# Kernel tuning notes

Measured on AMD Instinct MI355X. Metric: run time of the kernel, lower is better.

The kernel has to match this reference:

```python
import jax, jax.numpy as jnp
import numpy as np

N = 50000          # nodes
E = 1250000        # edges (no self loops in raw data)
H = 2              # heads
C = 32             # out channels per head
DIN = 64           # dim_node
ED = 16            # edge_dim
G = 16             # graphs in batch
NC = 5             # num classes
SLOPE = 0.2        # GATConv leaky_relu negative_slope


def _glorot(key, shape):
    fan = shape[0] if len(shape) == 2 else shape[-1]
    return jax.random.normal(key, shape, jnp.float32) * (1.0 / np.sqrt(fan))


def setup_inputs() -> dict:
    key = jax.random.key(0)
    ks = jax.random.split(key, 24)
    x = jax.random.normal(ks[0], (N, DIN), jnp.float32)
    dst = jax.random.randint(ks[1], (E,), 0, N)
    off = jax.random.randint(ks[2], (E,), 1, N)
    src = (dst + off) % N  # guarantees src != dst (PyG removes self loops before re-adding)
    edge_index = jnp.stack([src, dst]).astype(jnp.int32)
    edge_attr = jax.random.normal(ks[3], (E, ED), jnp.float32)
    batch = jnp.sort(jax.random.randint(ks[4], (N,), 0, G)).astype(jnp.int32)
    inp = dict(x=x, edge_index=edge_index, edge_attr=edge_attr, batch=batch)
    # layer 1: in=DIN, heads=H, out=C, concat -> H*C
    inp["W1"] = _glorot(ks[5], (DIN, H * C)); inp["asrc1"] = _glorot(ks[6], (H, C))
    inp["adst1"] = _glorot(ks[7], (H, C)); inp["We1"] = _glorot(ks[8], (ED, H * C))
    inp["ae1"] = _glorot(ks[9], (H, C)); inp["b1"] = jnp.zeros((H * C,), jnp.float32)
    # layer 2: in=H*C, heads=H, out=C, concat
    inp["W2"] = _glorot(ks[10], (H * C, H * C)); inp["asrc2"] = _glorot(ks[11], (H, C))
    inp["adst2"] = _glorot(ks[12], (H, C)); inp["We2"] = _glorot(ks[13], (ED, H * C))
    inp["ae2"] = _glorot(ks[14], (H, C)); inp["b2"] = jnp.zeros((H * C,), jnp.float32)
    # layer 3: in=H*C, heads=1, out=C, concat=False
    inp["W3"] = _glorot(ks[15], (H * C, C)); inp["asrc3"] = _glorot(ks[16], (1, C))
    inp["adst3"] = _glorot(ks[17], (1, C)); inp["We3"] = _glorot(ks[18], (ED, C))
    inp["ae3"] = _glorot(ks[19], (1, C)); inp["b3"] = jnp.zeros((C,), jnp.float32)
    # ffn: Linear(C, NC) + softmax (dropout is identity in eval)
    inp["Wf"] = _glorot(ks[20], (C, NC)); inp["bf"] = jnp.zeros((NC,), jnp.float32)
    return inp


def _gat_layer(h_in, src, dst, eattr, W, asrc, adst, We, ae, b, heads, out, concat):
    n = h_in.shape[0]
    h = (h_in @ W).reshape(n, heads, out)                      # [N,H,C]
    s_src = jnp.einsum('nhc,hc->nh', h, asrc)                  # per-node src scores
    s_dst = jnp.einsum('nhc,hc->nh', h, adst)
    he = (eattr @ We).reshape(-1, heads, out)                  # [E,H,C]
    s_e = jnp.einsum('ehc,hc->eh', he, ae)
    logit = jax.nn.leaky_relu(s_src[src] + s_dst[dst] + s_e, SLOPE)  # [E,H]
    m = jax.ops.segment_max(logit, dst, num_segments=n)
    ex = jnp.exp(logit - m[dst])
    den = jax.ops.segment_sum(ex, dst, num_segments=n)
    alpha = ex / (den[dst] + 1e-16)                            # segment softmax per dst node
    agg = jax.ops.segment_sum(h[src] * alpha[..., None], dst, num_segments=n)  # [N,H,C]
    out_x = agg.reshape(n, heads * out) if concat else agg.mean(axis=1)
    return out_x + b


def _gat_forward(x, edge_index, edge_attr, batch,
                 W1, asrc1, adst1, We1, ae1, b1,
                 W2, asrc2, adst2, We2, ae2, b2,
                 W3, asrc3, adst3, We3, ae3, b3,
                 Wf, bf):
    src, dst = edge_index[0], edge_index[1]
    n = x.shape[0]
    # add_self_loops with fill_value='mean': self-loop edge_attr = mean of incoming edge_attr
    deg = jax.ops.segment_sum(jnp.ones((src.shape[0],), x.dtype), dst, num_segments=n)
    self_attr = jax.ops.segment_sum(edge_attr, dst, num_segments=n) / jnp.maximum(deg, 1.0)[:, None]
    loop = jnp.arange(n, dtype=src.dtype)
    src_a = jnp.concatenate([src, loop])
    dst_a = jnp.concatenate([dst, loop])
    eattr_a = jnp.concatenate([edge_attr, self_attr], axis=0)

    h = jax.nn.relu(_gat_layer(x, src_a, dst_a, eattr_a, W1, asrc1, adst1, We1, ae1, b1, H, C, True))
    h = jax.nn.relu(_gat_layer(h, src_a, dst_a, eattr_a, W2, asrc2, adst2, We2, ae2, b2, H, C, True))
    h = jax.nn.relu(_gat_layer(h, src_a, dst_a, eattr_a, W3, asrc3, adst3, We3, ae3, b3, 1, C, False))

    # global mean pool per graph
    cnt = jax.ops.segment_sum(jnp.ones((n,), h.dtype), batch, num_segments=G)
    pooled = jax.ops.segment_sum(h, batch, num_segments=G) / jnp.maximum(cnt, 1.0)[:, None]
    # ffn: Dropout (identity at eval) -> Linear -> Softmax(dim=1)
    return jax.nn.softmax(pooled @ Wf + bf, axis=1)


def reference(x, edge_index, edge_attr, batch,
              W1, asrc1, adst1, We1, ae1, b1,
              W2, asrc2, adst2, We2, ae2, b2,
              W3, asrc3, adst3, We3, ae3, b3,
              Wf, bf):
    return _gat_forward(x, edge_index, edge_attr, batch,
                        W1, asrc1, adst1, We1, ae1, b1,
                        W2, asrc2, adst2, We2, ae2, b2,
                        W3, asrc3, adst3, We3, ae3, b3,
                        Wf, bf)
```

## Files before the change

### kernel.cpp

```cpp
#include <hip/hip_runtime.h>
#include <math.h>

#define NN 50000
#define EE 1250000
#define GG 16
#define NCLS 5
#define NBIN 391
#define BINSHIFT 7
#define CAPB 3900

constexpr size_t AL(size_t x){ return (x + 255) & ~size_t(255); }
constexpr size_t OFF_DEG    = 0;
constexpr size_t OFF_ROWPTR = OFF_DEG + AL((size_t)NN*4);
constexpr size_t OFF_CURSOR = OFF_ROWPTR + AL((size_t)(NN+1)*4);
constexpr size_t OFF_SRCS   = OFF_CURSOR + AL((size_t)NN*4);
constexpr size_t OFF_SE12   = OFF_SRCS + AL((size_t)EE*2);
constexpr size_t OFF_SE34   = OFF_SE12 + AL((size_t)EE*4);
constexpr size_t OFF_SE5    = OFF_SE34 + AL((size_t)EE*4);
constexpr size_t OFF_SSRC   = OFF_SE5 + AL((size_t)EE*2);
constexpr size_t OFF_SDST   = OFF_SSRC + AL((size_t)NN*2*4);
constexpr size_t OFF_STAG   = OFF_SDST + AL((size_t)NN*2*4);
constexpr size_t OFF_BUFH   = OFF_STAG + AL((size_t)NBIN*CAPB*16);
constexpr size_t OFF_BUFO   = OFF_BUFH + AL((size_t)NN*32*4);
constexpr size_t OFF_WEFF   = OFF_BUFO + AL((size_t)NN*64*4);
constexpr size_t OFF_POOL   = OFF_WEFF + AL(80*4);

__device__ __forceinline__ float leaky(float x){ return x > 0.f ? x : 0.2f*x; }
__device__ __forceinline__ unsigned rne_bf16(float x){
    unsigned u = __float_as_uint(x);
    return (u + 0x7FFFu + ((u >> 16) & 1u)) >> 16;
}
__device__ __forceinline__ float bf16lo(unsigned p){ return __uint_as_float(p << 16); }
__device__ __forceinline__ float bf16hi(unsigned p){ return __uint_as_float(p & 0xFFFF0000u); }

__global__ void weff_kernel(const float* __restrict__ We1, const float* __restrict__ ae1,
                            const float* __restrict__ We2, const float* __restrict__ ae2,
                            const float* __restrict__ We3, const float* __restrict__ ae3,
                            float* __restrict__ weff){
    int t = threadIdx.x;
    if (t >= 80) return;
    int j = t >> 4, d = t & 15;
    const float* We; const float* ae; int hc, h;
    if (j == 0){ We = We1; ae = ae1; hc = 64; h = 0; }
    else if (j == 1){ We = We1; ae = ae1; hc = 64; h = 1; }
    else if (j == 2){ We = We2; ae = ae2; hc = 64; h = 0; }
    else if (j == 3){ We = We2; ae = ae2; hc = 64; h = 1; }
    else { We = We3; ae = ae3; hc = 32; h = 0; }
    float s = 0.f;
    for (int c = 0; c < 32; ++c) s += We[d*hc + h*32 + c] * ae[h*32 + c];
    weff[j*16 + d] = s;
}

__global__ void binit_kernel(int* __restrict__ bincursor){
    int b = blockIdx.x*256 + threadIdx.x;
    if (b < NBIN) bincursor[b] = b*CAPB;
}

__global__ void binA_kernel(const int* __restrict__ src, const int* __restrict__ dst,
                            const float* __restrict__ eattr, const float* __restrict__ weff,
                            int* __restrict__ bincursor, int4* __restrict__ staging, int nE){
    __shared__ int lcount[NBIN];
    __shared__ int lbase[NBIN];
    __shared__ float w[80];
    int tid = threadIdx.x;
    if (tid < 80) w[tid] = weff[tid];
    for (int i = tid; i < NBIN; i += 1024) lcount[i] = 0;
    __syncthreads();
    int base = blockIdx.x * 2048;
    int w0[2], bn[2], idx[2]; unsigned p01[2], p23[2], p4[2];
    #pragma unroll
    for (int k = 0; k < 2; ++k){
        int i = base + k*1024 + tid;
        if (i < nE){
            int d = dst[i];
            int s = src[i];
            bn[k]  = d >> BINSHIFT;
            w0[k]  = s | ((d & 127) << 16);
            const float4* row = (const float4*)(eattr + (size_t)i*16);
            float4 a0 = row[0], a1 = row[1], a2 = row[2], a3 = row[3];
            float a[16] = {a0.x,a0.y,a0.z,a0.w, a1.x,a1.y,a1.z,a1.w,
                           a2.x,a2.y,a2.z,a2.w, a3.x,a3.y,a3.z,a3.w};
            float sj[5];
            #pragma unroll
            for (int j = 0; j < 5; ++j){
                float s2 = 0.f;
                #pragma unroll
                for (int d2 = 0; d2 < 16; ++d2) s2 += a[d2]*w[j*16+d2];
                sj[j] = s2;
            }
            p01[k] = rne_bf16(sj[0]) | (rne_bf16(sj[1]) << 16);
            p23[k] = rne_bf16(sj[2]) | (rne_bf16(sj[3]) << 16);
            p4[k]  = rne_bf16(sj[4]);
            idx[k] = atomicAdd(&lcount[bn[k]], 1);
        } else bn[k] = -1;
    }
    __syncthreads();
    for (int i = tid; i < NBIN; i += 1024)
        lbase[i] = atomicAdd(&bincursor[i], lcount[i]);
    __syncthreads();
    #pragma unroll
    for (int k = 0; k < 2; ++k)
        if (bn[k] >= 0)
            staging[lbase[bn[k]] + idx[k]] = make_int4(w0[k], (int)p01[k], (int)p23[k], (int)p4[k]);
}

__global__ void hist_kernel(const int4* __restrict__ staging, const int* __restrict__ bincursor,
                            int* __restrict__ deg, int nN){
    __shared__ int lcnt[128];
    int b = blockIdx.x;
    int tid = threadIdx.x;
    if (tid < 128) lcnt[tid] = 0;
    __syncthreads();
    int base = b*CAPB;
    int cnt = bincursor[b] - base;
    for (int k = tid; k < cnt; k += 256)
        atomicAdd(&lcnt[staging[base + k].x >> 16], 1);
    __syncthreads();
    int lo = b << BINSHIFT;
    if (tid < 128 && lo + tid < nN) deg[lo + tid] = lcnt[tid];
}

__global__ void bsum_kernel(const int* __restrict__ deg, int* __restrict__ bsum, int nN){
    __shared__ int s[1024];
    int tid = threadIdx.x;
    int i = blockIdx.x*1024 + tid;
    s[tid] = (i < nN) ? deg[i] : 0;
    __syncthreads();
    for (int off = 512; off > 0; off >>= 1){
        if (tid < off) s[tid] += s[tid+off];
        __syncthreads();
    }
    if (tid == 0) bsum[blockIdx.x] = s[0];
}

__global__ void bscan_kernel(const int* __restrict__ bsum, int* __restrict__ boff,
                             int* __restrict__ rowptr, int nB, int nN){
    int lane = threadIdx.x;
    int v = (lane < nB) ? bsum[lane] : 0;
    int incl = v;
    #pragma unroll
    for (int off = 1; off < 64; off <<= 1){
        int t = __shfl_up(incl, off);
        if (lane >= off) incl += t;
    }
    if (lane < nB) boff[lane] = incl - v;
    if (lane == 63) rowptr[nN] = incl;
}

__global__ void wptr_kernel(const int* __restrict__ deg, const int* __restrict__ boff,
                            int* __restrict__ rowptr, int nN){
    __shared__ int s[1024];
    int tid = threadIdx.x;
    int i = blockIdx.x*1024 + tid;
    int v = (i < nN) ? deg[i] : 0;
    s[tid] = v;
    __syncthreads();
    for (int off = 1; off < 1024; off <<= 1){
        int t = (tid >= off) ? s[tid-off] : 0;
        __syncthreads();
        s[tid] += t;
        __syncthreads();
    }
    if (i < nN) rowptr[i] = boff[blockIdx.x] + s[tid] - v;
}

__global__ void binB_kernel(const int* __restrict__ rowptr, const int4* __restrict__ staging,
                            unsigned short* __restrict__ srcs, unsigned* __restrict__ se12,
                            unsigned* __restrict__ se34, unsigned short* __restrict__ se5, int nN){
    __shared__ int4 lout[CAPB];
    __shared__ int lcnt[128];
    int b = blockIdx.x;
    int lo = b << BINSHIFT;
    int hi = min(lo + 128, nN);
    int r0 = rowptr[lo], r1 = rowptr[hi];
    int cnt = r1 - r0;
    int sbase = b*CAPB;
    int tid = threadIdx.x;
    if (tid < 128) lcnt[tid] = 0;
    __syncthreads();
    for (int k = tid; k < cnt; k += 1024){
        int4 v = staging[sbase + k];
        int dl = v.x >> 16;
        int rank = atomicAdd(&lcnt[dl], 1);
        int target = rowptr[lo + dl] - r0 + rank;
        v.x &= 0xFFFF;
        if (target < CAPB) lout[target] = v;
        else {
            srcs[r0 + target] = (unsigned short)v.x;
            se12[r0 + target] = (unsigned)v.y;
            se34[r0 + target] = (unsigned)v.z;
            se5[r0 + target]  = (unsigned short)v.w;
        }
    }
    __syncthreads();
    int m = min(cnt, CAPB);
    for (int k = tid; k < m; k += 1024){
        int4 v = lout[k];
        srcs[r0 + k] = (unsigned short)v.x;
        se12[r0 + k] = (unsigned)v.y;
        se34[r0 + k] = (unsigned)v.z;
        se5[r0 + k]  = (unsigned short)v.w;
    }
}

template<int OUTC>
__global__ void transform_kernel(const float* __restrict__ in, const float* __restrict__ W,
                                 const float* __restrict__ asrc, const float* __restrict__ adst,
                                 unsigned* __restrict__ hout2, float* __restrict__ ssrc,
                                 float* __restrict__ sdst, int nN){
    constexpr int R = 256/OUTC;
    __shared__ float Ws[64*OUTC];
    __shared__ float ins[R*64];
    int tid = threadIdx.x;
    for (int i = tid; i < 64*OUTC; i += 256) Ws[i] = W[i];
    int base = blockIdx.x * R;
    for (int i = tid; i < R*64; i += 256){
        int n = base + i/64;
        ins[i] = (n < nN) ? in[(size_t)n*64 + (i & 63)] : 0.f;
    }
    __syncthreads();
    int r = tid / OUTC, c = tid % OUTC;
    int n = base + r;
    float acc = 0.f;
    #pragma unroll
    for (int d = 0; d < 64; ++d) acc += ins[r*64 + d] * Ws[d*OUTC + c];
    float ps = acc * asrc[c];
    float pd = acc * adst[c];
    #pragma unroll
    for (int m = 1; m <= 16; m <<= 1){ ps += __shfl_xor(ps, m); pd += __shfl_xor(pd, m); }
    float accN = __shfl_xor(acc, 1);
    if (n < nN){
        if ((c & 1) == 0){
            unsigned pk = rne_bf16(acc) | (rne_bf16(accN) << 16);
            hout2[(size_t)n*(OUTC/2) + (c >> 1)] = pk;
        }
        constexpr int HEADS = OUTC/32;
        if ((c & 31) == 0){
            int h = c >> 5;
            ssrc[n*HEADS + h] = ps;
            sdst[n*HEADS + h] = pd;
        }
    }
}

template<int OUTC>
__global__ void agg_kernel(const int* __restrict__ rowptr, const unsigned short* __restrict__ srcs,
                           const unsigned* __restrict__ sePa, const unsigned short* __restrict__ sePb,
                           const float* __restrict__ ssrc, const float* __restrict__ sdst,
                           const unsigned* __restrict__ hbuf2, const float* __restrict__ bias,
                           float* __restrict__ outbuf, int nN){
    constexpr int HEADS = OUTC/32;
    int wid = threadIdx.x >> 6;
    int lane = threadIdx.x & 63;
    int n = blockIdx.x*4 + wid;
    if (n >= nN) return;
    int row_start = rowptr[n], row_end = rowptr[n+1];
    int degn = row_end - row_start;
    float sd0 = sdst[n*HEADS + 0];
    float sd1 = (HEADS == 2) ? sdst[n*HEADS + 1] : 0.f;

    const uint2* hb2 = (const uint2*)hbuf2;
    float acc0=0.f, acc1=0.f, acc2=0.f, acc3=0.f, den=0.f, sspL=0.f;

    int h, lc;
    if (HEADS == 2){ int s = lane >> 3; h = s & 1; lc = lane & 7; }
    else           { h = 0; lc = lane & 7; }

    if (HEADS == 2){
        int eoff = lane >> 1, hp = lane & 1;
        int q0 = (lane >> 4);
        float sdh_p = hp ? sd1 : sd0;
        for (int p0 = row_start; p0 < row_end; p0 += 32){
            int myp = p0 + eoff;
            unsigned wpk = 0;
            if (myp < row_end){
                int srcreg = srcs[myp];
                unsigned pk = sePa[myp];
                float e = hp ? bf16hi(pk) : bf16lo(pk);
                sspL += e;
                float sh = ssrc[2*srcreg + hp];
                float wv = __expf(leaky(sh + sdh_p + e));
                wpk = (unsigned)srcreg | (rne_bf16(wv) << 16);
            }
            int cnt = min(32, row_end - p0);
            for (int qq = q0; qq < cnt; qq += 4){
                unsigned u = __shfl(wpk, 2*qq + h);
                int sj = u & 0xFFFF;
                float wj = __uint_as_float(u & 0xFFFF0000u);
                den += wj;
                uint2 hv = hb2[(size_t)sj*16 + h*8 + lc];
                acc0 += wj * bf16lo(hv.x);
                acc1 += wj * bf16hi(hv.x);
                acc2 += wj * bf16lo(hv.y);
                acc3 += wj * bf16hi(hv.y);
            }
        }
        #pragma unroll
        for (int m = 2; m < 64; m <<= 1) sspL += __shfl_xor(sspL, m);
        float ssh = __shfl(sspL, h);
        #pragma unroll
        for (int m = 16; m < 64; m <<= 1){
            acc0 += __shfl_xor(acc0, m); acc1 += __shfl_xor(acc1, m);
            acc2 += __shfl_xor(acc2, m); acc3 += __shfl_xor(acc3, m);
            den  += __shfl_xor(den, m);
        }
        float invdeg = 1.f / (float)max(degn, 1);
        float srh = ssrc[2*n + h];
        float sdh = h ? sd1 : sd0;
        float wself = __expf(leaky(srh + sdh + ssh*invdeg));
        uint2 hv = hb2[(size_t)n*16 + h*8 + lc];
        acc0 += wself * bf16lo(hv.x); acc1 += wself * bf16hi(hv.x);
        acc2 += wself * bf16lo(hv.y); acc3 += wself * bf16hi(hv.y);
        den += wself;
        if (lane < 16){
            float inv = 1.f / (den + 1e-16f);
            int idx4 = h*8 + lc;
            float4 o;
            o.x = fmaxf(acc0*inv + bias[4*idx4+0], 0.f);
            o.y = fmaxf(acc1*inv + bias[4*idx4+1], 0.f);
            o.z = fmaxf(acc2*inv + bias[4*idx4+2], 0.f);
            o.w = fmaxf(acc3*inv + bias[4*idx4+3], 0.f);
            ((float4*)outbuf)[(size_t)n*16 + idx4] = o;
        }
    } else {
        int q0 = lane >> 3;
        for (int p0 = row_start; p0 < row_end; p0 += 64){
            int myp = p0 + lane;
            unsigned wpk = 0;
            if (myp < row_end){
                int srcreg = srcs[myp];
                float e = __uint_as_float(((unsigned)sePb[myp]) << 16);
                sspL += e;
                float wv = __expf(leaky(ssrc[srcreg] + sd0 + e));
                wpk = (unsigned)srcreg | (rne_bf16(wv) << 16);
            }
            int cnt = min(64, row_end - p0);
            for (int qq = q0; qq < cnt; qq += 8){
                unsigned u = __shfl(wpk, qq);
                int sj = u & 0xFFFF;
                float wj = __uint_as_float(u & 0xFFFF0000u);
                den += wj;
                uint2 hv = hb2[(size_t)sj*8 + lc];
                acc0 += wj * bf16lo(hv.x);
                acc1 += wj * bf16hi(hv.x);
                acc2 += wj * bf16lo(hv.y);
                acc3 += wj * bf16hi(hv.y);
            }
        }
        #pragma unroll
        for (int m = 1; m < 64; m <<= 1) sspL += __shfl_xor(sspL, m);
        float ssh = sspL;
        #pragma unroll
        for (int m = 8; m < 64; m <<= 1){
            acc0 += __shfl_xor(acc0, m); acc1 += __shfl_xor(acc1, m);
            acc2 += __shfl_xor(acc2, m); acc3 += __shfl_xor(acc3, m);
            den  += __shfl_xor(den, m);
        }
        float invdeg = 1.f / (float)max(degn, 1);
        float wself = __expf(leaky(ssrc[n] + sd0 + ssh*invdeg));
        uint2 hv = hb2[(size_t)n*8 + lc];
        acc0 += wself * bf16lo(hv.x); acc1 += wself * bf16hi(hv.x);
        acc2 += wself * bf16lo(hv.y); acc3 += wself * bf16hi(hv.y);
        den += wself;
        if (lane < 8){
            float inv = 1.f / (den + 1e-16f);
            float4 o;
            o.x = fmaxf(acc0*inv + bias[4*lc+0], 0.f);
            o.y = fmaxf(acc1*inv + bias[4*lc+1], 0.f);
            o.z = fmaxf(acc2*inv + bias[4*lc+2], 0.f);
            o.w = fmaxf(acc3*inv + bias[4*lc+3], 0.f);
            ((float4*)outbuf)[(size_t)n*8 + lc] = o;
        }
    }
}

__global__ void pool_kernel(const float* __restrict__ h3, const int* __restrict__ batch,
                            float* __restrict__ pool, float* __restrict__ cnt, int nN){
    __shared__ float accs[GG*32];
    __shared__ float acccnt[GG];
    int tid = threadIdx.x;
    for (int i = tid; i < GG*32; i += 256) accs[i] = 0.f;
    if (tid < GG) acccnt[tid] = 0.f;
    __syncthreads();
    int r = tid >> 5, c = tid & 31;
    int base = blockIdx.x * 512;
    int end = min(base + 512, nN);
    for (int n = base + r; n < end; n += 8){
        int g = batch[n];
        atomicAdd(&accs[g*32 + c], h3[(size_t)n*32 + c]);
        if (c == 0) atomicAdd(&acccnt[g], 1.f);
    }
    __syncthreads();
    for (int i = tid; i < GG*32; i += 256) atomicAdd(&pool[i], accs[i]);
    if (tid < GG) atomicAdd(&cnt[tid], acccnt[tid]);
}

__global__ void final_kernel(const float* __restrict__ pool, const float* __restrict__ cnt,
                             const float* __restrict__ Wf, const float* __restrict__ bf,
                             float* __restrict__ out){
    int g = threadIdx.x;
    if (g >= GG) return;
    float ic = 1.f / fmaxf(cnt[g], 1.f);
    float lg[NCLS];
    #pragma unroll
    for (int k = 0; k < NCLS; ++k) lg[k] = bf[k];
    for (int c = 0; c < 32; ++c){
        float v = pool[g*32 + c] * ic;
        #pragma unroll
        for (int k = 0; k < NCLS; ++k) lg[k] += v * Wf[c*NCLS + k];
    }
    float mx = lg[0];
    #pragma unroll
    for (int k = 1; k < NCLS; ++k) mx = fmaxf(mx, lg[k]);
    float sum = 0.f, ex[NCLS];
    #pragma unroll
    for (int k = 0; k < NCLS; ++k){ ex[k] = expf(lg[k] - mx); sum += ex[k]; }
    #pragma unroll
    for (int k = 0; k < NCLS; ++k) out[g*NCLS + k] = ex[k]/sum;
}

extern "C" void kernel_launch(void* const* d_in, const int* in_sizes, int n_in,
                              void* d_out, int out_size, void* d_ws, size_t ws_size,
                              hipStream_t stream){
    const float* x     = (const float*)d_in[0];
    const int*   eidx  = (const int*)d_in[1];
    const float* eattr = (const float*)d_in[2];
    const int*   batch = (const int*)d_in[3];
    const float* W1 = (const float*)d_in[4];  const float* asrc1 = (const float*)d_in[5];
    const float* adst1 = (const float*)d_in[6]; const float* We1 = (const float*)d_in[7];
    const float* ae1 = (const float*)d_in[8];  const float* b1 = (const float*)d_in[9];
    const float* W2 = (const float*)d_in[10]; const float* asrc2 = (const float*)d_in[11];
    const float* adst2 = (const float*)d_in[12]; const float* We2 = (const float*)d_in[13];
    const float* ae2 = (const float*)d_in[14]; const float* b2 = (const float*)d_in[15];
    const float* W3 = (const float*)d_in[16]; const float* asrc3 = (const float*)d_in[17];
    const float* adst3 = (const float*)d_in[18]; const float* We3 = (const float*)d_in[19];
    const float* ae3 = (const float*)d_in[20]; const float* b3 = (const float*)d_in[21];
    const float* Wf = (const float*)d_in[22]; const float* bf = (const float*)d_in[23];
    float* out = (float*)d_out;

    char* ws = (char*)d_ws;
    int*   deg    = (int*)(ws + OFF_DEG);
    int*   rowptr = (int*)(ws + OFF_ROWPTR);
    int*   curs   = (int*)(ws + OFF_CURSOR);
    unsigned short* srcs = (unsigned short*)(ws + OFF_SRCS);
    unsigned* se12 = (unsigned*)(ws + OFF_SE12);
    unsigned* se34 = (unsigned*)(ws + OFF_SE34);
    unsigned short* se5 = (unsigned short*)(ws + OFF_SE5);
    float* ssrc   = (float*)(ws + OFF_SSRC);
    float* sdst   = (float*)(ws + OFF_SDST);
    int4*  staging = (int4*)(ws + OFF_STAG);
    unsigned* bufH = (unsigned*)(ws + OFF_BUFH);
    float* bufO   = (float*)(ws + OFF_BUFO);
    float* weff   = (float*)(ws + OFF_WEFF);
    float* pool   = (float*)(ws + OFF_POOL);
    float* cnt    = pool + GG*32;

    int* bincursor = curs;
    int* bsum      = curs + 512;
    int* boff      = curs + 1024;

    const int* srcA = eidx;
    const int* dstA = eidx + EE;

    hipMemsetAsync(pool, 0, (GG*32 + GG)*4, stream);

    weff_kernel<<<1, 128, 0, stream>>>(We1, ae1, We2, ae2, We3, ae3, weff);
    binit_kernel<<<(NBIN+255)/256, 256, 0, stream>>>(bincursor);
    binA_kernel<<<(EE + 2047)/2048, 1024, 0, stream>>>(srcA, dstA, eattr, weff, bincursor, staging, EE);
    hist_kernel<<<NBIN, 256, 0, stream>>>(staging, bincursor, deg, NN);
    int sgrid = (NN + 1023)/1024;
    bsum_kernel<<<sgrid, 1024, 0, stream>>>(deg, bsum, NN);
    bscan_kernel<<<1, 64, 0, stream>>>(bsum, boff, rowptr, sgrid, NN);
    wptr_kernel<<<sgrid, 1024, 0, stream>>>(deg, boff, rowptr, NN);
    binB_kernel<<<NBIN, 1024, 0, stream>>>(rowptr, staging, srcs, se12, se34, se5, NN);

    int ngrid4 = (NN + 3)/4;
    int ngrid8 = (NN + 7)/8;
    transform_kernel<64><<<ngrid4, 256, 0, stream>>>(x, W1, asrc1, adst1, bufH, ssrc, sdst, NN);
    agg_kernel<64><<<ngrid4, 256, 0, stream>>>(rowptr, srcs, se12, nullptr,
                                               ssrc, sdst, bufH, b1, bufO, NN);
    transform_kernel<64><<<ngrid4, 256, 0, stream>>>(bufO, W2, asrc2, adst2, bufH, ssrc, sdst, NN);
    agg_kernel<64><<<ngrid4, 256, 0, stream>>>(rowptr, srcs, se34, nullptr,
                                               ssrc, sdst, bufH, b2, bufO, NN);
    transform_kernel<32><<<ngrid8, 256, 0, stream>>>(bufO, W3, asrc3, adst3, bufH, ssrc, sdst, NN);
    agg_kernel<32><<<ngrid4, 256, 0, stream>>>(rowptr, srcs, nullptr, se5,
                                               ssrc, sdst, bufH, b3, bufO, NN);
    pool_kernel<<<(NN + 511)/512, 256, 0, stream>>>(bufO, batch, pool, cnt, NN);
    final_kernel<<<1, 64, 0, stream>>>(pool, cnt, Wf, bf, out);
}
```

Baseline: 275.8 us.

## Fuse CSR build into bin kernels and split aggregation per head with head-major layout

Derives rowptr from per-bin counts inside binB, computing a local histogram and prefix scan there and prefix-summing bin totals in one small kernel. This replaces the separate hist/bsum/bscan/wptr kernels and the deg buffer, and merges binit into weff. The transform output and attention scores are stored head-major. Aggregation runs as one kernel per head, so each gather touches a contiguous per-head slice with a single code path. Layers 1 and 2 now launch twice as many aggregation kernels and re-read the CSR once per head.

```diff
diff --git a/kernel.cpp b/kernel.cpp
--- a/kernel.cpp
+++ b/kernel.cpp
@@ -10,10 +10,9 @@
 #define CAPB 3900
 
 constexpr size_t AL(size_t x){ return (x + 255) & ~size_t(255); }
-constexpr size_t OFF_DEG    = 0;
-constexpr size_t OFF_ROWPTR = OFF_DEG + AL((size_t)NN*4);
-constexpr size_t OFF_CURSOR = OFF_ROWPTR + AL((size_t)(NN+1)*4);
-constexpr size_t OFF_SRCS   = OFF_CURSOR + AL((size_t)NN*4);
+constexpr size_t OFF_ROWPTR = 0;
+constexpr size_t OFF_CURS   = OFF_ROWPTR + AL((size_t)(NN+1)*4);
+constexpr size_t OFF_SRCS   = OFF_CURS + AL(4096);
 constexpr size_t OFF_SE12   = OFF_SRCS + AL((size_t)EE*2);
 constexpr size_t OFF_SE34   = OFF_SE12 + AL((size_t)EE*4);
 constexpr size_t OFF_SE5    = OFF_SE34 + AL((size_t)EE*4);
@@ -33,11 +32,12 @@
 __device__ __forceinline__ float bf16lo(unsigned p){ return __uint_as_float(p << 16); }
 __device__ __forceinline__ float bf16hi(unsigned p){ return __uint_as_float(p & 0xFFFF0000u); }
 
-__global__ void weff_kernel(const float* __restrict__ We1, const float* __restrict__ ae1,
-                            const float* __restrict__ We2, const float* __restrict__ ae2,
-                            const float* __restrict__ We3, const float* __restrict__ ae3,
-                            float* __restrict__ weff){
+__global__ void weffbinit_kernel(const float* __restrict__ We1, const float* __restrict__ ae1,
+                                 const float* __restrict__ We2, const float* __restrict__ ae2,
+                                 const float* __restrict__ We3, const float* __restrict__ ae3,
+                                 float* __restrict__ weff, int* __restrict__ bincursor){
     int t = threadIdx.x;
+    if (t < NBIN) bincursor[t] = t*CAPB;
     if (t >= 80) return;
     int j = t >> 4, d = t & 15;
     const float* We; const float* ae; int hc, h;
@@ -49,11 +49,6 @@
     float s = 0.f;
     for (int c = 0; c < 32; ++c) s += We[d*hc + h*32 + c] * ae[h*32 + c];
     weff[j*16 + d] = s;
-}
-
-__global__ void binit_kernel(int* __restrict__ bincursor){
-    int b = blockIdx.x*256 + threadIdx.x;
-    if (b < NBIN) bincursor[b] = b*CAPB;
 }
 
 __global__ void binA_kernel(const int* __restrict__ src, const int* __restrict__ dst,
@@ -104,97 +99,66 @@
             staging[lbase[bn[k]] + idx[k]] = make_int4(w0[k], (int)p01[k], (int)p23[k], (int)p4[k]);
 }
 
-__global__ void hist_kernel(const int4* __restrict__ staging, const int* __restrict__ bincursor,
-                            int* __restrict__ deg, int nN){
-    __shared__ int lcnt[128];
-    int b = blockIdx.x;
-    int tid = threadIdx.x;
-    if (tid < 128) lcnt[tid] = 0;
-    __syncthreads();
-    int base = b*CAPB;
-    int cnt = bincursor[b] - base;
-    for (int k = tid; k < cnt; k += 256)
-        atomicAdd(&lcnt[staging[base + k].x >> 16], 1);
-    __syncthreads();
-    int lo = b << BINSHIFT;
-    if (tid < 128 && lo + tid < nN) deg[lo + tid] = lcnt[tid];
-}
-
-__global__ void bsum_kernel(const int* __restrict__ deg, int* __restrict__ bsum, int nN){
-    __shared__ int s[1024];
-    int tid = threadIdx.x;
-    int i = blockIdx.x*1024 + tid;
-    s[tid] = (i < nN) ? deg[i] : 0;
-    __syncthreads();
-    for (int off = 512; off > 0; off >>= 1){
-        if (tid < off) s[tid] += s[tid+off];
-        __syncthreads();
-    }
-    if (tid == 0) bsum[blockIdx.x] = s[0];
-}
-
-__global__ void bscan_kernel(const int* __restrict__ bsum, int* __restrict__ boff,
-                             int* __restrict__ rowptr, int nB, int nN){
-    int lane = threadIdx.x;
-    int v = (lane < nB) ? bsum[lane] : 0;
-    int incl = v;
-    #pragma unroll
-    for (int off = 1; off < 64; off <<= 1){
-        int t = __shfl_up(incl, off);
-        if (lane >= off) incl += t;
-    }
-    if (lane < nB) boff[lane] = incl - v;
-    if (lane == 63) rowptr[nN] = incl;
-}
-
-__global__ void wptr_kernel(const int* __restrict__ deg, const int* __restrict__ boff,
-                            int* __restrict__ rowptr, int nN){
-    __shared__ int s[1024];
-    int tid = threadIdx.x;
-    int i = blockIdx.x*1024 + tid;
-    int v = (i < nN) ? deg[i] : 0;
+__global__ void binscan_kernel(const int* __restrict__ bincursor, int* __restrict__ binbase){
+    __shared__ int s[512];
+    int tid = threadIdx.x;
+    int v = (tid < NBIN) ? (bincursor[tid] - tid*CAPB) : 0;
     s[tid] = v;
     __syncthreads();
-    for (int off = 1; off < 1024; off <<= 1){
+    for (int off = 1; off < 512; off <<= 1){
         int t = (tid >= off) ? s[tid-off] : 0;
         __syncthreads();
         s[tid] += t;
         __syncthreads();
     }
-    if (i < nN) rowptr[i] = boff[blockIdx.x] + s[tid] - v;
-}
-
-__global__ void binB_kernel(const int* __restrict__ rowptr, const int4* __restrict__ staging,
+    if (tid < NBIN) binbase[tid] = s[tid] - v;
+}
+
+__global__ void binB_kernel(const int* __restrict__ bincursor, const int* __restrict__ binbase,
+                            const int4* __restrict__ staging,
                             unsigned short* __restrict__ srcs, unsigned* __restrict__ se12,
-                            unsigned* __restrict__ se34, unsigned short* __restrict__ se5, int nN){
+                            unsigned* __restrict__ se34, unsigned short* __restrict__ se5,
+                            int* __restrict__ rowptr, int nN){
     __shared__ int4 lout[CAPB];
     __shared__ int lcnt[128];
+    __shared__ int lpre[128];
     int b = blockIdx.x;
+    int sbase = b*CAPB;
+    int cnt = bincursor[b] - sbase;
+    int tid = threadIdx.x;
+    if (tid < 128) lcnt[tid] = 0;
+    __syncthreads();
+    for (int k = tid; k < cnt; k += 1024)
+        atomicAdd(&lcnt[staging[sbase + k].x >> 16], 1);
+    __syncthreads();
+    if (tid < 64){
+        int a0 = lcnt[2*tid], a1 = lcnt[2*tid+1];
+        int pair = a0 + a1, incl = pair;
+        #pragma unroll
+        for (int off = 1; off < 64; off <<= 1){
+            int t = __shfl_up(incl, off);
+            if (tid >= off) incl += t;
+        }
+        int base0 = incl - pair;
+        lpre[2*tid] = base0;
+        lpre[2*tid+1] = base0 + a0;
+    }
+    __syncthreads();
+    int r0 = binbase[b];
     int lo = b << BINSHIFT;
-    int hi = min(lo + 128, nN);
-    int r0 = rowptr[lo], r1 = rowptr[hi];
-    int cnt = r1 - r0;
-    int sbase = b*CAPB;
-    int tid = threadIdx.x;
+    if (tid < 128 && lo + tid < nN) rowptr[lo + tid] = r0 + lpre[tid];
+    if (b == NBIN-1 && tid == 0) rowptr[nN] = r0 + cnt;
     if (tid < 128) lcnt[tid] = 0;
     __syncthreads();
     for (int k = tid; k < cnt; k += 1024){
         int4 v = staging[sbase + k];
         int dl = v.x >> 16;
         int rank = atomicAdd(&lcnt[dl], 1);
-        int target = rowptr[lo + dl] - r0 + rank;
         v.x &= 0xFFFF;
-        if (target < CAPB) lout[target] = v;
-        else {
-            srcs[r0 + target] = (unsigned short)v.x;
-            se12[r0 + target] = (unsigned)v.y;
-            se34[r0 + target] = (unsigned)v.z;
-            se5[r0 + target]  = (unsigned short)v.w;
-        }
-    }
-    __syncthreads();
-    int m = min(cnt, CAPB);
-    for (int k = tid; k < m; k += 1024){
+        lout[lpre[dl] + rank] = v;
+    }
+    __syncthreads();
+    for (int k = tid; k < cnt; k += 1024){
         int4 v = lout[k];
         srcs[r0 + k] = (unsigned short)v.x;
         se12[r0 + k] = (unsigned)v.y;
@@ -230,147 +194,82 @@
     for (int m = 1; m <= 16; m <<= 1){ ps += __shfl_xor(ps, m); pd += __shfl_xor(pd, m); }
     float accN = __shfl_xor(acc, 1);
     if (n < nN){
+        int h = c >> 5;
         if ((c & 1) == 0){
             unsigned pk = rne_bf16(acc) | (rne_bf16(accN) << 16);
-            hout2[(size_t)n*(OUTC/2) + (c >> 1)] = pk;
-        }
-        constexpr int HEADS = OUTC/32;
+            hout2[((size_t)h*nN + n)*16 + ((c & 31) >> 1)] = pk;
+        }
         if ((c & 31) == 0){
-            int h = c >> 5;
-            ssrc[n*HEADS + h] = ps;
-            sdst[n*HEADS + h] = pd;
-        }
-    }
-}
-
-template<int OUTC>
-__global__ void agg_kernel(const int* __restrict__ rowptr, const unsigned short* __restrict__ srcs,
-                           const unsigned* __restrict__ sePa, const unsigned short* __restrict__ sePb,
-                           const float* __restrict__ ssrc, const float* __restrict__ sdst,
-                           const unsigned* __restrict__ hbuf2, const float* __restrict__ bias,
-                           float* __restrict__ outbuf, int nN){
-    constexpr int HEADS = OUTC/32;
+            ssrc[(size_t)h*nN + n] = ps;
+            sdst[(size_t)h*nN + n] = pd;
+        }
+    }
+}
+
+template<int MODE>
+__global__ void aggH_kernel(const int* __restrict__ rowptr, const unsigned short* __restrict__ srcs,
+                            const unsigned* __restrict__ sePa, const unsigned short* __restrict__ sePb,
+                            const float* __restrict__ ssrcH, const float* __restrict__ sdstH,
+                            const uint2* __restrict__ hb2, const float* __restrict__ bias,
+                            float4* __restrict__ outb, int ostride4, int nN){
     int wid = threadIdx.x >> 6;
     int lane = threadIdx.x & 63;
     int n = blockIdx.x*4 + wid;
     if (n >= nN) return;
     int row_start = rowptr[n], row_end = rowptr[n+1];
     int degn = row_end - row_start;
-    float sd0 = sdst[n*HEADS + 0];
-    float sd1 = (HEADS == 2) ? sdst[n*HEADS + 1] : 0.f;
-
-    const uint2* hb2 = (const uint2*)hbuf2;
-    float acc0=0.f, acc1=0.f, acc2=0.f, acc3=0.f, den=0.f, sspL=0.f;
-
-    int h, lc;
-    if (HEADS == 2){ int s = lane >> 3; h = s & 1; lc = lane & 7; }
-    else           { h = 0; lc = lane & 7; }
-
-    if (HEADS == 2){
-        int eoff = lane >> 1, hp = lane & 1;
-        int q0 = (lane >> 4);
-        float sdh_p = hp ? sd1 : sd0;
-        for (int p0 = row_start; p0 < row_end; p0 += 32){
-            int myp = p0 + eoff;
-            unsigned wpk = 0;
-            if (myp < row_end){
-                int srcreg = srcs[myp];
-                unsigned pk = sePa[myp];
-                float e = hp ? bf16hi(pk) : bf16lo(pk);
-                sspL += e;
-                float sh = ssrc[2*srcreg + hp];
-                float wv = __expf(leaky(sh + sdh_p + e));
-                wpk = (unsigned)srcreg | (rne_bf16(wv) << 16);
-            }
-            int cnt = min(32, row_end - p0);
-            for (int qq = q0; qq < cnt; qq += 4){
-                unsigned u = __shfl(wpk, 2*qq + h);
-                int sj = u & 0xFFFF;
-                float wj = __uint_as_float(u & 0xFFFF0000u);
-                den += wj;
-                uint2 hv = hb2[(size_t)sj*16 + h*8 + lc];
-                acc0 += wj * bf16lo(hv.x);
-                acc1 += wj * bf16hi(hv.x);
-                acc2 += wj * bf16lo(hv.y);
-                acc3 += wj * bf16hi(hv.y);
-            }
-        }
-        #pragma unroll
-        for (int m = 2; m < 64; m <<= 1) sspL += __shfl_xor(sspL, m);
-        float ssh = __shfl(sspL, h);
-        #pragma unroll
-        for (int m = 16; m < 64; m <<= 1){
-            acc0 += __shfl_xor(acc0, m); acc1 += __shfl_xor(acc1, m);
-            acc2 += __shfl_xor(acc2, m); acc3 += __shfl_xor(acc3, m);
-            den  += __shfl_xor(den, m);
-        }
-        float invdeg = 1.f / (float)max(degn, 1);
-        float srh = ssrc[2*n + h];
-        float sdh = h ? sd1 : sd0;
-        float wself = __expf(leaky(srh + sdh + ssh*invdeg));
-        uint2 hv = hb2[(size_t)n*16 + h*8 + lc];
-        acc0 += wself * bf16lo(hv.x); acc1 += wself * bf16hi(hv.x);
-        acc2 += wself * bf16lo(hv.y); acc3 += wself * bf16hi(hv.y);
-        den += wself;
-        if (lane < 16){
-            float inv = 1.f / (den + 1e-16f);
-            int idx4 = h*8 + lc;
-            float4 o;
-            o.x = fmaxf(acc0*inv + bias[4*idx4+0], 0.f);
-            o.y = fmaxf(acc1*inv + bias[4*idx4+1], 0.f);
-            o.z = fmaxf(acc2*inv + bias[4*idx4+2], 0.f);
-            o.w = fmaxf(acc3*inv + bias[4*idx4+3], 0.f);
-            ((float4*)outbuf)[(size_t)n*16 + idx4] = o;
-        }
-    } else {
-        int q0 = lane >> 3;
-        for (int p0 = row_start; p0 < row_end; p0 += 64){
-            int myp = p0 + lane;
-            unsigned wpk = 0;
-            if (myp < row_end){
-                int srcreg = srcs[myp];
-                float e = __uint_as_float(((unsigned)sePb[myp]) << 16);
-                sspL += e;
-                float wv = __expf(leaky(ssrc[srcreg] + sd0 + e));
-                wpk = (unsigned)srcreg | (rne_bf16(wv) << 16);
-            }
-            int cnt = min(64, row_end - p0);
-            for (int qq = q0; qq < cnt; qq += 8){
-                unsigned u = __shfl(wpk, qq);
-                int sj = u & 0xFFFF;
-                float wj = __uint_as_float(u & 0xFFFF0000u);
-                den += wj;
-                uint2 hv = hb2[(size_t)sj*8 + lc];
-                acc0 += wj * bf16lo(hv.x);
-                acc1 += wj * bf16hi(hv.x);
-                acc2 += wj * bf16lo(hv.y);
-                acc3 += wj * bf16hi(hv.y);
-            }
-        }
-        #pragma unroll
-        for (int m = 1; m < 64; m <<= 1) sspL += __shfl_xor(sspL, m);
-        float ssh = sspL;
-        #pragma unroll
-        for (int m = 8; m < 64; m <<= 1){
-            acc0 += __shfl_xor(acc0, m); acc1 += __shfl_xor(acc1, m);
-            acc2 += __shfl_xor(acc2, m); acc3 += __shfl_xor(acc3, m);
-            den  += __shfl_xor(den, m);
-        }
-        float invdeg = 1.f / (float)max(degn, 1);
-        float wself = __expf(leaky(ssrc[n] + sd0 + ssh*invdeg));
-        uint2 hv = hb2[(size_t)n*8 + lc];
-        acc0 += wself * bf16lo(hv.x); acc1 += wself * bf16hi(hv.x);
-        acc2 += wself * bf16lo(hv.y); acc3 += wself * bf16hi(hv.y);
-        den += wself;
-        if (lane < 8){
-            float inv = 1.f / (den + 1e-16f);
-            float4 o;
-            o.x = fmaxf(acc0*inv + bias[4*lc+0], 0.f);
-            o.y = fmaxf(acc1*inv + bias[4*lc+1], 0.f);
-            o.z = fmaxf(acc2*inv + bias[4*lc+2], 0.f);
-            o.w = fmaxf(acc3*inv + bias[4*lc+3], 0.f);
-            ((float4*)outbuf)[(size_t)n*8 + lc] = o;
-        }
+    float sdh = sdstH[n];
+    int q0 = lane >> 3, lc = lane & 7;
+
+    float acc0=0.f, acc1=0.f, acc2=0.f, acc3=0.f, den=0.f, ssp=0.f;
+    for (int p0 = row_start; p0 < row_end; p0 += 64){
+        int myp = p0 + lane;
+        unsigned wpk = 0;
+        if (myp < row_end){
+            int srcreg = srcs[myp];
+            float e;
+            if (MODE == 0)      e = __uint_as_float(((unsigned)sePb[myp]) << 16);
+            else if (MODE == 1) e = bf16lo(sePa[myp]);
+            else                e = bf16hi(sePa[myp]);
+            ssp += e;
+            float wv = __expf(leaky(ssrcH[srcreg] + sdh + e));
+            wpk = (unsigned)srcreg | (rne_bf16(wv) << 16);
+        }
+        int cnt2 = min(64, row_end - p0);
+        for (int qq = q0; qq < cnt2; qq += 8){
+            unsigned u = __shfl(wpk, qq);
+            int sj = u & 0xFFFF;
+            float wj = __uint_as_float(u & 0xFFFF0000u);
+            den += wj;
+            uint2 hv = hb2[(size_t)sj*8 + lc];
+            acc0 += wj * bf16lo(hv.x);
+            acc1 += wj * bf16hi(hv.x);
+            acc2 += wj * bf16lo(hv.y);
+            acc3 += wj * bf16hi(hv.y);
+        }
+    }
+    #pragma unroll
+    for (int m = 1; m < 64; m <<= 1) ssp += __shfl_xor(ssp, m);
+    #pragma unroll
+    for (int m = 8; m < 64; m <<= 1){
+        acc0 += __shfl_xor(acc0, m); acc1 += __shfl_xor(acc1, m);
+        acc2 += __shfl_xor(acc2, m); acc3 += __shfl_xor(acc3, m);
+        den  += __shfl_xor(den, m);
+    }
+    float invdeg = 1.f / (float)max(degn, 1);
+    float wself = __expf(leaky(ssrcH[n] + sdh + ssp*invdeg));
+    uint2 hv = hb2[(size_t)n*8 + lc];
+    acc0 += wself * bf16lo(hv.x); acc1 += wself * bf16hi(hv.x);
+    acc2 += wself * bf16lo(hv.y); acc3 += wself * bf16hi(hv.y);
+    den += wself;
+    if (lane < 8){
+        float inv = 1.f / (den + 1e-16f);
+        float4 o;
+        o.x = fmaxf(acc0*inv + bias[4*lc+0], 0.f);
+        o.y = fmaxf(acc1*inv + bias[4*lc+1], 0.f);
+        o.z = fmaxf(acc2*inv + bias[4*lc+2], 0.f);
+        o.w = fmaxf(acc3*inv + bias[4*lc+3], 0.f);
+        outb[(size_t)n*ostride4 + lc] = o;
     }
 }
 
@@ -439,9 +338,8 @@
     float* out = (float*)d_out;
 
     char* ws = (char*)d_ws;
-    int*   deg    = (int*)(ws + OFF_DEG);
     int*   rowptr = (int*)(ws + OFF_ROWPTR);
-    int*   curs   = (int*)(ws + OFF_CURSOR);
+    int*   curs   = (int*)(ws + OFF_CURS);
     unsigned short* srcs = (unsigned short*)(ws + OFF_SRCS);
     unsigned* se12 = (unsigned*)(ws + OFF_SE12);
     unsigned* se34 = (unsigned*)(ws + OFF_SE34);
@@ -456,35 +354,30 @@
     float* cnt    = pool + GG*32;
 
     int* bincursor = curs;
-    int* bsum      = curs + 512;
-    int* boff      = curs + 1024;
+    int* binbase   = curs + 512;
 
     const int* srcA = eidx;
     const int* dstA = eidx + EE;
 
     hipMemsetAsync(pool, 0, (GG*32 + GG)*4, stream);
 
-    weff_kernel<<<1, 128, 0, stream>>>(We1, ae1, We2, ae2, We3, ae3, weff);
-    binit_kernel<<<(NBIN+255)/256, 256, 0, stream>>>(bincursor);
+    weffbinit_kernel<<<1, 512, 0, stream>>>(We1, ae1, We2, ae2, We3, ae3, weff, bincursor);
     binA_kernel<<<(EE + 2047)/2048, 1024, 0, stream>>>(srcA, dstA, eattr, weff, bincursor, staging, EE);
-    hist_kernel<<<NBIN, 256, 0, stream>>>(staging, bincursor, deg, NN);
-    int sgrid = (NN + 1023)/1024;
-    bsum_kernel<<<sgrid, 1024, 0, stream>>>(deg, bsum, NN);
-    bscan_kernel<<<1, 64, 0, stream>>>(bsum, boff, rowptr, sgrid, NN);
-    wptr_kernel<<<sgrid, 1024, 0, stream>>>(deg, boff, rowptr, NN);
-    binB_kernel<<<NBIN, 1024, 0, stream>>>(rowptr, staging, srcs, se12, se34, se5, NN);
+    binscan_kernel<<<1, 512, 0, stream>>>(bincursor, binbase);
+    binB_kernel<<<NBIN, 1024, 0, stream>>>(bincursor, binbase, staging, srcs, se12, se34, se5, rowptr, NN);
 
     int ngrid4 = (NN + 3)/4;
     int ngrid8 = (NN + 7)/8;
+    const uint2* hb = (const uint2*)bufH;
+    float4* o4 = (float4*)bufO;
     transform_kernel<64><<<ngrid4, 256, 0, stream>>>(x, W1, asrc1, adst1, bufH, ssrc, sdst, NN);
-    agg_kernel<64><<<ngrid4, 256, 0, stream>>>(rowptr, srcs, se12, nullptr,
-                                               ssrc, sdst, bufH, b1, bufO, NN);
+    aggH_kernel<1><<<ngrid4, 256, 0, stream>>>(rowptr, srcs, se12, nullptr, ssrc,      sdst,      hb,          b1,      o4,     16, NN);
+    aggH_kernel<2><<<ngrid4, 256, 0, stream>>>(rowptr, srcs, se12, nullptr, ssrc + NN, sdst + NN, hb + NN*8,   b1 + 32, o4 + 8, 16, NN);
     transform_kernel<64><<<ngrid4, 256, 0, stream>>>(bufO, W2, asrc2, adst2, bufH, ssrc, sdst, NN);
-    agg_kernel<64><<<ngrid4, 256, 0, stream>>>(rowptr, srcs, se34, nullptr,
-                                               ssrc, sdst, bufH, b2, bufO, NN);
+    aggH_kernel<1><<<ngrid4, 256, 0, stream>>>(rowptr, srcs, se34, nullptr, ssrc,      sdst,      hb,          b2,      o4,     16, NN);
+    aggH_kernel<2><<<ngrid4, 256, 0, stream>>>(rowptr, srcs, se34, nullptr, ssrc + NN, sdst + NN, hb + NN*8,   b2 + 32, o4 + 8, 16, NN);
     transform_kernel<32><<<ngrid8, 256, 0, stream>>>(bufO, W3, asrc3, adst3, bufH, ssrc, sdst, NN);
-    agg_kernel<32><<<ngrid4, 256, 0, stream>>>(rowptr, srcs, nullptr, se5,
-                                               ssrc, sdst, bufH, b3, bufO, NN);
+    aggH_kernel<0><<<ngrid4, 256, 0, stream>>>(rowptr, srcs, nullptr, se5, ssrc, sdst, hb, b3, o4, 8, NN);
     pool_kernel<<<(NN + 511)/512, 256, 0, stream>>>(bufO, batch, pool, cnt, NN);
     final_kernel<<<1, 64, 0, stream>>>(pool, cnt, Wf, bf, out);
 }
```

After: 299.2 us. 8.5% more time.
